# Performance work log

Measured on AMD Instinct MI355X. Metric: run time of the kernel, lower is better.

Reference implementation:

```python
import jax, jax.numpy as jnp
import numpy as np

N = 100000   # nodes
E = 1600000  # edges (before self-loops)
C = 128      # num_node_features == graph_hidden_channels (residuals require equality)
NHID = 512
NOUT = 256
B = 512      # number of graphs in the batch
BN_EPS = 1e-5


def setup_inputs() -> dict:
    key = jax.random.key(0)
    ks = list(jax.random.split(key, 32))
    k = iter(ks)

    def w(shape, fan_in):
        return jax.random.normal(next(k), shape, jnp.float32) * (1.0 / np.sqrt(fan_in))

    inp = {}
    inp["x"] = jax.random.normal(next(k), (N, C), jnp.float32)
    inp["edge_index"] = jax.random.randint(next(k), (2, E), 0, N, jnp.int32)
    inp["batch"] = jnp.sort(jax.random.randint(next(k), (N,), 0, B, jnp.int32))
    # three GCN layers: lin weight [C,C], bias [C], BN gamma/beta
    for i in (1, 2, 3):
        inp[f"W{i}"] = w((C, C), C)
        inp[f"b{i}"] = jnp.zeros((C,), jnp.float32)
        inp[f"g{i}"] = jnp.ones((C,), jnp.float32)
        inp[f"be{i}"] = jnp.zeros((C,), jnp.float32)
    # GAT (1 head)
    inp["Wa"] = w((C, C), C)
    inp["asrc"] = w((C,), C)
    inp["adst"] = w((C,), C)
    inp["ba"] = jnp.zeros((C,), jnp.float32)
    inp["ga"] = jnp.ones((C,), jnp.float32)
    inp["bea"] = jnp.zeros((C,), jnp.float32)
    # MLP head
    inp["Wh1"] = w((C, NHID), C)
    inp["bh1"] = jnp.zeros((NHID,), jnp.float32)
    inp["Wm0"] = w((NHID, NHID), NHID)
    inp["bm0"] = jnp.zeros((NHID,), jnp.float32)
    inp["Wm1"] = w((NHID, NHID), NHID)
    inp["bm1"] = jnp.zeros((NHID,), jnp.float32)
    inp["Wo"] = w((NHID, NOUT), NHID)
    inp["bo"] = jnp.zeros((NOUT,), jnp.float32)
    return inp


def _add_self_loops(edge_index):
    loops = jnp.arange(N, dtype=edge_index.dtype)
    src = jnp.concatenate([edge_index[0], loops])
    dst = jnp.concatenate([edge_index[1], loops])
    return src, dst


def _gcn(x, src, dst, W, b):
    # PyG GCNConv: add self-loops, D^-1/2 (A+I) D^-1/2 (x W) + b
    deg = jax.ops.segment_sum(jnp.ones_like(dst, jnp.float32), dst, num_segments=N)
    dinv = jax.lax.rsqrt(jnp.maximum(deg, 1.0))
    norm = dinv[src] * dinv[dst]                      # [E+N]
    h = x @ W                                         # [N,C]
    msg = h[src] * norm[:, None]                      # gather + scale
    return jax.ops.segment_sum(msg, dst, num_segments=N) + b


def _gat(x, src, dst, W, asrc, adst, b):
    # PyG GATConv, heads=1: self-loops, alpha = softmax_dst(leaky_relu(a_s.h_j + a_d.h_i))
    h = x @ W                                         # [N,C]
    es = (h * asrc).sum(-1)                           # [N]
    ed = (h * adst).sum(-1)
    e = jax.nn.leaky_relu(es[src] + ed[dst], 0.2)     # [E+N]
    m = jax.ops.segment_max(e, dst, num_segments=N)
    ex = jnp.exp(e - m[dst])
    s = jax.ops.segment_sum(ex, dst, num_segments=N)
    alpha = ex / (s[dst] + 1e-16)
    out = jax.ops.segment_sum(h[src] * alpha[:, None], dst, num_segments=N)
    return out + b


def _bn(h, g, be):
    # BatchNorm in training mode: biased batch stats over node dim
    m = h.mean(0)
    v = ((h - m) ** 2).mean(0)
    return (h - m) * jax.lax.rsqrt(v + BN_EPS) * g + be


def reference(x, edge_index, batch,
              W1, b1, g1, be1, W2, b2, g2, be2, W3, b3, g3, be3,
              Wa, asrc, adst, ba, ga, bea,
              Wh1, bh1, Wm0, bm0, Wm1, bm1, Wo, bo):
    src, dst = _add_self_loops(edge_index)
    x = jax.nn.relu(_bn(_gcn(x, src, dst, W1, b1), g1, be1)) + x
    x = jax.nn.relu(_bn(_gcn(x, src, dst, W2, b2), g2, be2)) + x
    x = jax.nn.relu(_bn(_gcn(x, src, dst, W3, b3), g3, be3)) + x
    x = jax.nn.relu(_bn(_gat(x, src, dst, Wa, asrc, adst, ba), ga, bea)) + x
    # global mean pool over graphs
    sums = jax.ops.segment_sum(x, batch, num_segments=B)
    cnt = jax.ops.segment_sum(jnp.ones((N,), jnp.float32), batch, num_segments=B)
    x = sums / jnp.maximum(cnt, 1.0)[:, None]         # [B,C]
    x = jax.nn.relu(x @ Wh1 + bh1)
    x = jax.nn.relu(x @ Wm0 + bm0)
    x = jax.nn.relu(x @ Wm1 + bm1)
    return x @ Wo + bo                                # [B,NOUT]
```

## Files before the change

### kernel.cpp

```cpp
#include <hip/hip_runtime.h>

#define N_NODES 100000
#define N_EDGES 1600000
#define CCH     128
#define BG      512
#define NHID    512
#define NOUT    256
#define BN_EPS  1e-5f

typedef __attribute__((ext_vector_type(8))) short s16x8;
typedef __attribute__((ext_vector_type(4))) float f32x4;

static __device__ __forceinline__ float leaky(float x) { return x > 0.f ? x : 0.2f * x; }
static __device__ __forceinline__ uint32_t bfr16(float x) {
  uint32_t u = __float_as_uint(x);
  u += 0x7fffu + ((u >> 16) & 1u);
  return u >> 16;
}
static __device__ __forceinline__ uint32_t pack2(float a, float b) {
  return bfr16(a) | (bfr16(b) << 16);
}
static __device__ __forceinline__ float blo(uint32_t u) { return __uint_as_float(u << 16); }
static __device__ __forceinline__ float bhi(uint32_t u) { return __uint_as_float(u & 0xffff0000u); }

__global__ void hist_kernel(const int* __restrict__ dst, int* __restrict__ indeg) {
  int e = blockIdx.x * 256 + threadIdx.x;
  if (e < N_EDGES) atomicAdd(&indeg[dst[e]], 1);
}

__global__ __launch_bounds__(256) void scan_chunks(const int* __restrict__ indeg,
                                                   int* __restrict__ rowstart,
                                                   int* __restrict__ chunksum) {
  int tid = threadIdx.x;
  int base = blockIdx.x * 1024 + tid * 4;
  int4 v;
  if (base + 3 < N_NODES) {
    v = *(const int4*)(indeg + base);
  } else {
    v.x = (base + 0 < N_NODES) ? indeg[base + 0] : 0;
    v.y = (base + 1 < N_NODES) ? indeg[base + 1] : 0;
    v.z = (base + 2 < N_NODES) ? indeg[base + 2] : 0;
    v.w = (base + 3 < N_NODES) ? indeg[base + 3] : 0;
  }
  int s = v.x + v.y + v.z + v.w;
  __shared__ int ss[256];
  ss[tid] = s;
  __syncthreads();
  for (int off = 1; off < 256; off <<= 1) {
    int t = (tid >= off) ? ss[tid - off] : 0;
    __syncthreads();
    ss[tid] += t;
    __syncthreads();
  }
  int excl = ss[tid] - s;
  if (base + 0 < N_NODES) rowstart[base + 0] = excl;
  if (base + 1 < N_NODES) rowstart[base + 1] = excl + v.x;
  if (base + 2 < N_NODES) rowstart[base + 2] = excl + v.x + v.y;
  if (base + 3 < N_NODES) rowstart[base + 3] = excl + v.x + v.y + v.z;
  if (tid == 255) chunksum[blockIdx.x] = ss[255];
}

__global__ void scan_sums(int* __restrict__ chunksum, int nch) {
  __shared__ int ss[128];
  int tid = threadIdx.x;
  int v = (tid < nch) ? chunksum[tid] : 0;
  ss[tid] = v;
  __syncthreads();
  for (int off = 1; off < 128; off <<= 1) {
    int t = (tid >= off) ? ss[tid - off] : 0;
    __syncthreads();
    ss[tid] += t;
    __syncthreads();
  }
  if (tid < nch) chunksum[tid] = ss[tid] - v;
}

__global__ void scan_add_dinv(int* __restrict__ rowstart, const int* __restrict__ chunksum,
                              const int* __restrict__ indeg, float* __restrict__ dinv) {
  int i = blockIdx.x * 256 + threadIdx.x;
  if (i < N_NODES) {
    rowstart[i] += chunksum[i >> 10];
    dinv[i] = rsqrtf((float)(indeg[i] + 1));
  } else if (i == N_NODES) {
    rowstart[N_NODES] = N_EDGES;
  }
}

__global__ void scatter_edges(const int* __restrict__ src, const int* __restrict__ dst,
                              const int* __restrict__ rowstart, int* __restrict__ cursor,
                              const float* __restrict__ dinv, int2* __restrict__ csr_sw) {
  int e = blockIdx.x * 256 + threadIdx.x;
  if (e < N_EDGES) {
    int d = dst[e];
    int s = src[e];
    int p = rowstart[d] + atomicAdd(&cursor[d], 1);
    float w = dinv[s] * dinv[d];
    csr_sw[p] = make_int2(s, __float_as_int(w));
  }
}

__global__ void prep_kernel(const float2* __restrict__ x2, uint32_t* __restrict__ xb,
                            const float* __restrict__ W1, const float* __restrict__ W2,
                            const float* __restrict__ W3, const float* __restrict__ W4,
                            unsigned short* __restrict__ Wp1, unsigned short* __restrict__ Wp2,
                            unsigned short* __restrict__ Wp3, unsigned short* __restrict__ Wp4) {
  int b = blockIdx.x;
  if (b < 25000) {
    size_t idx = (size_t)b * 256 + threadIdx.x;
    float2 v = x2[idx];
    xb[idx] = pack2(v.x, v.y);
    return;
  }
  int pb = b - 25000;
  int wsel = pb >> 3;
  int t = (pb & 7) * 256 + threadIdx.x;
  const float* W = (wsel == 0) ? W1 : (wsel == 1) ? W2 : (wsel == 2) ? W3 : W4;
  unsigned short* Wp = (wsel == 0) ? Wp1 : (wsel == 1) ? Wp2 : (wsel == 2) ? Wp3 : Wp4;
  int lane = t & 63;
  int ks = (t >> 6) & 3;
  int nt = t >> 8;
  int c = nt * 16 + (lane & 15);
  int kb = ks * 32 + (lane >> 4) * 8;
#pragma unroll
  for (int i = 0; i < 8; ++i)
    Wp[(size_t)t * 8 + i] = (unsigned short)bfr16(W[(size_t)(kb + i) * 128 + c]);
}

template <int FUSE>
__global__ __launch_bounds__(256) void gemm_mfma(uint32_t* __restrict__ xbm,
                                                 const float* __restrict__ aggf,
                                                 const float* __restrict__ stats,
                                                 const float* __restrict__ gamma,
                                                 const float* __restrict__ beta,
                                                 const unsigned short* __restrict__ Wp,
                                                 uint32_t* __restrict__ Hb,
                                                 int M) {
  __shared__ float scs[128], bcs[128];
  if (FUSE) {
    int t = threadIdx.x;
    if (t < 128) {
      const float n_inv = 1.f / (float)N_NODES;
      float m = stats[t] * n_inv;
      float v = stats[128 + t] * n_inv - m * m;
      float s = gamma[t] * rsqrtf(v + BN_EPS);
      scs[t] = s;
      bcs[t] = beta[t] - m * s;
    }
    __syncthreads();
  }
  int wave = threadIdx.x >> 6, lane = threadIdx.x & 63;
  int row0 = blockIdx.x * 128 + wave * 32;
  int r = lane & 15, g = lane >> 4;

  f32x4 acc[2][8];
#pragma unroll
  for (int mt = 0; mt < 2; ++mt)
#pragma unroll
    for (int nt = 0; nt < 8; ++nt) acc[mt][nt] = (f32x4){0.f, 0.f, 0.f, 0.f};

  s16x8 a[2][4];
#pragma unroll
  for (int mt = 0; mt < 2; ++mt) {
    int row = row0 + mt * 16 + r;
    bool v = row < M;
    if (FUSE) {
#pragma unroll
      for (int ks = 0; ks < 4; ++ks) {
        int ch = ks * 32 + g * 8;
        s16x8 af = {0, 0, 0, 0, 0, 0, 0, 0};
        if (v) {
          const float4* ap = (const float4*)(aggf + (size_t)row * 128 + ch);
          float4 a0 = ap[0], a1 = ap[1];
          uint4 xo = *(const uint4*)(xbm + (size_t)row * 64 + (ch >> 1));
          float aa[8] = {a0.x, a0.y, a0.z, a0.w, a1.x, a1.y, a1.z, a1.w};
          float xold[8] = {blo(xo.x), bhi(xo.x), blo(xo.y), bhi(xo.y),
                           blo(xo.z), bhi(xo.z), blo(xo.w), bhi(xo.w)};
          uint32_t pk[4];
#pragma unroll
          for (int jj = 0; jj < 4; ++jj) {
            float r0v = fmaxf(fmaf(aa[2 * jj],     scs[ch + 2 * jj],     bcs[ch + 2 * jj]),     0.f) + xold[2 * jj];
            float r1v = fmaxf(fmaf(aa[2 * jj + 1], scs[ch + 2 * jj + 1], bcs[ch + 2 * jj + 1]), 0.f) + xold[2 * jj + 1];
            pk[jj] = pack2(r0v, r1v);
          }
          uint4 st = make_uint4(pk[0], pk[1], pk[2], pk[3]);
          *(uint4*)(xbm + (size_t)row * 64 + (ch >> 1)) = st;
          af = *(s16x8*)&st;
        }
        a[mt][ks] = af;
      }
    } else {
      const unsigned short* ap = (const unsigned short*)xbm + (size_t)row * 128 + g * 8;
#pragma unroll
      for (int ks = 0; ks < 4; ++ks) {
        s16x8 af = {0, 0, 0, 0, 0, 0, 0, 0};
        if (v) af = *(const s16x8*)(ap + ks * 32);
        a[mt][ks] = af;
      }
    }
  }
#pragma unroll
  for (int ks = 0; ks < 4; ++ks) {
#pragma unroll
    for (int nt = 0; nt < 8; ++nt) {
      s16x8 bfr = *(const s16x8*)(Wp + ((size_t)(nt * 4 + ks) * 64 + lane) * 8);
      acc[0][nt] = __builtin_amdgcn_mfma_f32_16x16x32_bf16(a[0][ks], bfr, acc[0][nt], 0, 0, 0);
      acc[1][nt] = __builtin_amdgcn_mfma_f32_16x16x32_bf16(a[1][ks], bfr, acc[1][nt], 0, 0, 0);
    }
  }
#pragma unroll
  for (int mt = 0; mt < 2; ++mt) {
#pragma unroll
    for (int nt = 0; nt < 8; ++nt) {
#pragma unroll
      for (int reg = 0; reg < 4; ++reg) {
        float v0 = acc[mt][nt][reg];
        float v1 = __shfl_xor(v0, 1);
        int row = row0 + mt * 16 + (lane >> 4) * 4 + reg;
        int col = nt * 16 + (lane & 15);
        if (!(lane & 1) && row < M)
          Hb[(size_t)row * 64 + (col >> 1)] = pack2(v0, v1);
      }
    }
  }
}

template <int GAT>
__global__ __launch_bounds__(256) void agg_kernel(const uint2* __restrict__ Hb2,
                                                  const int* __restrict__ rowstart,
                                                  const int2* __restrict__ pack,
                                                  const float* __restrict__ dinv,
                                                  const float* __restrict__ es,
                                                  const float* __restrict__ ed,
                                                  float4* __restrict__ agg4,
                                                  float* __restrict__ stats) {
  int tid = threadIdx.x;
  int lane = tid & 63;
  int hl = lane & 31;
  int half = lane >> 5;
  int gw = (blockIdx.x * 256 + tid) >> 6;
  int nw = (gridDim.x * 256) >> 6;
  float s0 = 0, s1 = 0, s2 = 0, s3 = 0, q0 = 0, q1 = 0, q2 = 0, q3 = 0;
  for (int pi = gw; pi < N_NODES / 2; pi += nw) {
    int n = 2 * pi + half;
    int e0 = rowstart[n], e1 = rowstart[n + 1];
    int len = e1 - e0;
    int G = (len + 3) >> 2;
    int Gmax = max(G, __shfl_xor(G, 32));
    int ecl = (len > 0) ? (e1 - 1) : 0;
    float edi = 0.f, selfw, fscale = 1.f;
    if (GAT) {
      edi = ed[n];
      float wself = __expf(leaky(es[n] + edi));
      float wsum = (hl == 0) ? wself : 0.f;
      for (int e = e0 + hl; e < e1; e += 32)
        wsum += __expf(leaky(__int_as_float(pack[e].y) + edi));
#pragma unroll
      for (int off = 16; off; off >>= 1) wsum += __shfl_xor(wsum, off);
      fscale = 1.f / (wsum + 1e-16f);
      selfw = wself;
    } else {
      float di = dinv[n];
      selfw = di * di;
    }
#define EDGEW(py, ok) (GAT ? ((ok) ? __expf(leaky(__int_as_float(py) + edi)) : 0.f) \
                           : ((ok) ? __int_as_float(py) : 0.f))
    uint2 hs = Hb2[(size_t)n * 32 + hl];
    float c0 = blo(hs.x) * selfw, c1 = bhi(hs.x) * selfw;
    float c2 = blo(hs.y) * selfw, c3 = bhi(hs.y) * selfw;

    if (Gmax > 0) {
      uint2 rA0, rA1, rA2, rA3;
      float wA0, wA1, wA2, wA3;
      int iB0 = 0, iB1 = 0, iB2 = 0, iB3 = 0;
      float wB0 = 0, wB1 = 0, wB2 = 0, wB3 = 0;
      {
        int e = e0;
        int2 pa = pack[e < e1 ? e : ecl];
        int2 pb = pack[e + 1 < e1 ? e + 1 : ecl];
        int2 pc = pack[e + 2 < e1 ? e + 2 : ecl];
        int2 pd = pack[e + 3 < e1 ? e + 3 : ecl];
        wA0 = EDGEW(pa.y, e < e1);
        wA1 = EDGEW(pb.y, e + 1 < e1);
        wA2 = EDGEW(pc.y, e + 2 < e1);
        wA3 = EDGEW(pd.y, e + 3 < e1);
        rA0 = Hb2[(size_t)pa.x * 32 + hl];
        rA1 = Hb2[(size_t)pb.x * 32 + hl];
        rA2 = Hb2[(size_t)pc.x * 32 + hl];
        rA3 = Hb2[(size_t)pd.x * 32 + hl];
      }
      if (Gmax > 1) {
        int e = e0 + 4;
        int2 pa = pack[e < e1 ? e : ecl];
        int2 pb = pack[e + 1 < e1 ? e + 1 : ecl];
        int2 pc = pack[e + 2 < e1 ? e + 2 : ecl];
        int2 pd = pack[e + 3 < e1 ? e + 3 : ecl];
        iB0 = pa.x; wB0 = EDGEW(pa.y, e < e1);
        iB1 = pb.x; wB1 = EDGEW(pb.y, e + 1 < e1);
        iB2 = pc.x; wB2 = EDGEW(pc.y, e + 2 < e1);
        iB3 = pd.x; wB3 = EDGEW(pd.y, e + 3 < e1);
      }
      for (int g = 0; g < Gmax; ++g) {
        uint2 rB0, rB1, rB2, rB3;
        int nI0, nI1, nI2, nI3;
        float nw0, nw1, nw2, nw3;
        if (g + 1 < Gmax) {
          rB0 = Hb2[(size_t)iB0 * 32 + hl];
          rB1 = Hb2[(size_t)iB1 * 32 + hl];
          rB2 = Hb2[(size_t)iB2 * 32 + hl];
          rB3 = Hb2[(size_t)iB3 * 32 + hl];
        }
        if (g + 2 < Gmax) {
          int e = e0 + (g + 2) * 4;
          int2 pa = pack[e < e1 ? e : ecl];
          int2 pb = pack[e + 1 < e1 ? e + 1 : ecl];
          int2 pc = pack[e + 2 < e1 ? e + 2 : ecl];
          int2 pd = pack[e + 3 < e1 ? e + 3 : ecl];
          nI0 = pa.x; nw0 = EDGEW(pa.y, e < e1);
          nI1 = pb.x; nw1 = EDGEW(pb.y, e + 1 < e1);
          nI2 = pc.x; nw2 = EDGEW(pc.y, e + 2 < e1);
          nI3 = pd.x; nw3 = EDGEW(pd.y, e + 3 < e1);
        }
        c0 = fmaf(blo(rA0.x), wA0, c0); c1 = fmaf(bhi(rA0.x), wA0, c1);
        c2 = fmaf(blo(rA0.y), wA0, c2); c3 = fmaf(bhi(rA0.y), wA0, c3);
        c0 = fmaf(blo(rA1.x), wA1, c0); c1 = fmaf(bhi(rA1.x), wA1, c1);
        c2 = fmaf(blo(rA1.y), wA1, c2); c3 = fmaf(bhi(rA1.y), wA1, c3);
        c0 = fmaf(blo(rA2.x), wA2, c0); c1 = fmaf(bhi(rA2.x), wA2, c1);
        c2 = fmaf(blo(rA2.y), wA2, c2); c3 = fmaf(bhi(rA2.y), wA2, c3);
        c0 = fmaf(blo(rA3.x), wA3, c0); c1 = fmaf(bhi(rA3.x), wA3, c1);
        c2 = fmaf(blo(rA3.y), wA3, c2); c3 = fmaf(bhi(rA3.y), wA3, c3);
        rA0 = rB0; rA1 = rB1; rA2 = rB2; rA3 = rB3;
        wA0 = wB0; wA1 = wB1; wA2 = wB2; wA3 = wB3;
        iB0 = nI0; iB1 = nI1; iB2 = nI2; iB3 = nI3;
        wB0 = nw0; wB1 = nw1; wB2 = nw2; wB3 = nw3;
      }
    }
#undef EDGEW
    if (GAT) { c0 *= fscale; c1 *= fscale; c2 *= fscale; c3 *= fscale; }
    agg4[(size_t)n * 32 + hl] = make_float4(c0, c1, c2, c3);
    s0 += c0; s1 += c1; s2 += c2; s3 += c3;
    q0 += c0 * c0; q1 += c1 * c1; q2 += c2 * c2; q3 += c3 * c3;
  }
  s0 += __shfl_xor(s0, 32); s1 += __shfl_xor(s1, 32);
  s2 += __shfl_xor(s2, 32); s3 += __shfl_xor(s3, 32);
  q0 += __shfl_xor(q0, 32); q1 += __shfl_xor(q1, 32);
  q2 += __shfl_xor(q2, 32); q3 += __shfl_xor(q3, 32);
  __shared__ float red[4][128];
  int w = tid >> 6;
  if (half == 0) {
    red[w][4 * hl + 0] = s0; red[w][4 * hl + 1] = s1;
    red[w][4 * hl + 2] = s2; red[w][4 * hl + 3] = s3;
  }
  __syncthreads();
  if (w == 0) {
    float a = red[0][2 * lane] + red[1][2 * lane] + red[2][2 * lane] + red[3][2 * lane];
    float b = red[0][2 * lane + 1] + red[1][2 * lane + 1] + red[2][2 * lane + 1] + red[3][2 * lane + 1];
    atomicAdd(&stats[2 * lane], a);
    atomicAdd(&stats[2 * lane + 1], b);
  }
  __syncthreads();
  if (half == 0) {
    red[w][4 * hl + 0] = q0; red[w][4 * hl + 1] = q1;
    red[w][4 * hl + 2] = q2; red[w][4 * hl + 3] = q3;
  }
  __syncthreads();
  if (w == 0) {
    float a = red[0][2 * lane] + red[1][2 * lane] + red[2][2 * lane] + red[3][2 * lane];
    float b = red[0][2 * lane + 1] + red[1][2 * lane + 1] + red[2][2 * lane + 1] + red[3][2 * lane + 1];
    atomicAdd(&stats[128 + 2 * lane], a);
    atomicAdd(&stats[128 + 2 * lane + 1], b);
  }
}

__global__ __launch_bounds__(256) void compute_esed(const uint32_t* __restrict__ Hb,
                                                    const float* __restrict__ asrc,
                                                    const float* __restrict__ adst,
                                                    float* __restrict__ es, float* __restrict__ ed) {
  int lane = threadIdx.x & 63;
  int gwave = (blockIdx.x * 256 + threadIdx.x) >> 6;
  if (gwave >= N_NODES) return;
  float2 av = ((const float2*)asrc)[lane];
  float2 dv = ((const float2*)adst)[lane];
  uint32_t hv = Hb[(size_t)gwave * 64 + lane];
  float hx = blo(hv), hy = bhi(hv);
  float e_s = hx * av.x + hy * av.y;
  float e_d = hx * dv.x + hy * dv.y;
  for (int off = 32; off; off >>= 1) {
    e_s += __shfl_down(e_s, off);
    e_d += __shfl_down(e_d, off);
  }
  if (lane == 0) { es[gwave] = e_s; ed[gwave] = e_d; }
}

__global__ void gat_pack_kernel(int2* __restrict__ sw, const float* __restrict__ es) {
  int e = blockIdx.x * 256 + threadIdx.x;
  if (e < N_EDGES) {
    int2 v = sw[e];
    v.y = __float_as_int(es[v.x]);
    sw[e] = v;
  }
}

__global__ void graph_starts(const int* __restrict__ batch, int* __restrict__ gstart) {
  int n = blockIdx.x * 256 + threadIdx.x;
  if (n >= N_NODES) return;
  int b = batch[n];
  int bp = (n == 0) ? -1 : batch[n - 1];
  for (int g = bp + 1; g <= b; ++g) gstart[g] = n;
  if (n == N_NODES - 1) {
    for (int g = b + 1; g <= BG; ++g) gstart[g] = N_NODES;
  }
}

__global__ __launch_bounds__(256) void pool_bn(const float* __restrict__ aggf,
                                               const uint32_t* __restrict__ xb,
                                               const float* __restrict__ stats,
                                               const float* __restrict__ gamma,
                                               const float* __restrict__ beta,
                                               const int* __restrict__ gstart,
                                               float* __restrict__ pooled) {
  int g = blockIdx.x;
  int c = threadIdx.x & 127;
  int half = threadIdx.x >> 7;
  const float n_inv = 1.f / (float)N_NODES;
  float m = stats[c] * n_inv;
  float v = stats[128 + c] * n_inv - m * m;
  float sc = gamma[c] * rsqrtf(v + BN_EPS);
  float bc = beta[c] - m * sc;
  int s = gstart[g], e = gstart[g + 1];
  float acc = 0.f;
  for (int n = s + half; n < e; n += 2) {
    float a = aggf[(size_t)n * 128 + c];
    uint32_t u = xb[(size_t)n * 64 + (c >> 1)];
    float xo = (c & 1) ? bhi(u) : blo(u);
    acc += fmaxf(fmaf(a, sc, bc), 0.f) + xo;
  }
  __shared__ float red[256];
  red[threadIdx.x] = acc;
  __syncthreads();
  if (half == 0) {
    float vsum = red[c] + red[128 + c];
    int cnt = e - s;
    pooled[(size_t)g * 128 + c] = vsum / fmaxf((float)cnt, 1.f);
  }
}

template <int RELU, int BIAS>
__global__ __launch_bounds__(256) void gemm_f32(const float* __restrict__ A,
                                                const float* __restrict__ W,
                                                const float* __restrict__ bias,
                                                float* __restrict__ Cmat,
                                                int M, int K, int N) {
  __shared__ float As[32][128];
  __shared__ float Bs[32][128];
  int tid = threadIdx.x;
  int row0 = blockIdx.x * 128, col0 = blockIdx.y * 128;
  int tx = tid & 15, ty = tid >> 4;
  float acc[8][8];
#pragma unroll
  for (int i = 0; i < 8; ++i)
#pragma unroll
    for (int j = 0; j < 8; ++j) acc[i][j] = 0.f;

  for (int k0 = 0; k0 < K; k0 += 32) {
    {
      int r = tid >> 1;
      int kseg = (tid & 1) * 16;
      bool valid = (row0 + r) < M;
      const float* ap = A + (size_t)(row0 + r) * K + k0 + kseg;
#pragma unroll
      for (int q = 0; q < 4; ++q) {
        float4 v;
        if (valid) v = *(const float4*)(ap + q * 4);
        else { v.x = v.y = v.z = v.w = 0.f; }
        As[kseg + q * 4 + 0][r] = v.x;
        As[kseg + q * 4 + 1][r] = v.y;
        As[kseg + q * 4 + 2][r] = v.z;
        As[kseg + q * 4 + 3][r] = v.w;
      }
    }
    {
      int kk = tid >> 3;
      int seg = (tid & 7) * 16;
      const float* wp = W + (size_t)(k0 + kk) * N + col0 + seg;
#pragma unroll
      for (int q = 0; q < 4; ++q)
        *(float4*)&Bs[kk][seg + q * 4] = *(const float4*)(wp + q * 4);
    }
    __syncthreads();
#pragma unroll
    for (int kk = 0; kk < 32; ++kk) {
      float4 a0 = *(const float4*)&As[kk][ty * 4];
      float4 a1 = *(const float4*)&As[kk][64 + ty * 4];
      float4 b0 = *(const float4*)&Bs[kk][tx * 4];
      float4 b1 = *(const float4*)&Bs[kk][64 + tx * 4];
      float av[8] = {a0.x, a0.y, a0.z, a0.w, a1.x, a1.y, a1.z, a1.w};
      float bv[8] = {b0.x, b0.y, b0.z, b0.w, b1.x, b1.y, b1.z, b1.w};
#pragma unroll
      for (int i = 0; i < 8; ++i)
#pragma unroll
        for (int j = 0; j < 8; ++j) acc[i][j] = fmaf(av[i], bv[j], acc[i][j]);
    }
    __syncthreads();
  }
#pragma unroll
  for (int i = 0; i < 8; ++i) {
    int r = row0 + ((i < 4) ? (ty * 4 + i) : (64 + ty * 4 + i - 4));
    if (r >= M) continue;
#pragma unroll
    for (int j = 0; j < 8; ++j) {
      int c = col0 + ((j < 4) ? (tx * 4 + j) : (64 + tx * 4 + j - 4));
      float v = acc[i][j];
      if (BIAS) v += bias[c];
      if (RELU) v = fmaxf(v, 0.f);
      Cmat[(size_t)r * N + c] = v;
    }
  }
}

extern "C" void kernel_launch(void* const* d_in, const int* in_sizes, int n_in,
                              void* d_out, int out_size, void* d_ws, size_t ws_size,
                              hipStream_t stream) {
  const float* x_in  = (const float*)d_in[0];
  const int*   eidx  = (const int*)d_in[1];
  const int*   batch = (const int*)d_in[2];
  const float* W1 = (const float*)d_in[3];
  const float* g1 = (const float*)d_in[5];
  const float* be1 = (const float*)d_in[6];
  const float* W2 = (const float*)d_in[7];
  const float* g2 = (const float*)d_in[9];
  const float* be2 = (const float*)d_in[10];
  const float* W3 = (const float*)d_in[11];
  const float* g3 = (const float*)d_in[13];
  const float* be3 = (const float*)d_in[14];
  const float* Wa = (const float*)d_in[15];
  const float* asrc = (const float*)d_in[16];
  const float* adst = (const float*)d_in[17];
  const float* ga = (const float*)d_in[19];
  const float* bea = (const float*)d_in[20];
  const float* Wh1 = (const float*)d_in[21];
  const float* bh1 = (const float*)d_in[22];
  const float* Wm0 = (const float*)d_in[23];
  const float* bm0 = (const float*)d_in[24];
  const float* Wm1 = (const float*)d_in[25];
  const float* bm1 = (const float*)d_in[26];
  const float* Wo = (const float*)d_in[27];
  const float* bo = (const float*)d_in[28];

  const int* src = eidx;
  const int* dst = eidx + N_EDGES;

  char* p = (char*)d_ws;
  auto alloc = [&](size_t bytes) {
    char* r = p;
    p += (bytes + 255) & ~(size_t)255;
    return r;
  };
  uint32_t* Hb     = (uint32_t*)alloc((size_t)N_NODES * 64 * 4);
  uint32_t* xb     = (uint32_t*)alloc((size_t)N_NODES * 64 * 4);
  float* agg       = (float*)alloc((size_t)N_NODES * CCH * 4);
  int2*  csr_sw    = (int2*)alloc((size_t)N_EDGES * 8);
  int*   rowstart  = (int*)alloc((size_t)(N_NODES + 1) * 4);
  int*   indeg     = (int*)alloc((size_t)2 * N_NODES * 4);
  int*   cursor    = indeg + N_NODES;
  float* dinv      = (float*)alloc((size_t)N_NODES * 4);
  float* es        = (float*)alloc((size_t)N_NODES * 4);
  float* ed        = (float*)alloc((size_t)N_NODES * 4);
  int*   chunksum  = (int*)alloc(128 * 4);
  float* stats     = (float*)alloc(4 * 256 * 4);
  int*   gstart    = (int*)alloc((BG + 1) * 4);
  float* pooled    = (float*)alloc((size_t)BG * CCH * 4);
  float* m1        = (float*)alloc((size_t)BG * NHID * 4);
  float* m2        = (float*)alloc((size_t)BG * NHID * 4);
  unsigned short* Wp1 = (unsigned short*)alloc(2048 * 8 * 2);
  unsigned short* Wp2 = (unsigned short*)alloc(2048 * 8 * 2);
  unsigned short* Wp3 = (unsigned short*)alloc(2048 * 8 * 2);
  unsigned short* Wp4 = (unsigned short*)alloc(2048 * 8 * 2);

  hipMemsetAsync(indeg, 0, (size_t)2 * N_NODES * 4, stream);
  hipMemsetAsync(stats, 0, 4 * 256 * 4, stream);

  hist_kernel<<<(N_EDGES + 255) / 256, 256, 0, stream>>>(dst, indeg);
  scan_chunks<<<98, 256, 0, stream>>>(indeg, rowstart, chunksum);
  scan_sums<<<1, 128, 0, stream>>>(chunksum, 98);
  scan_add_dinv<<<(N_NODES + 256) / 256, 256, 0, stream>>>(rowstart, chunksum, indeg, dinv);
  scatter_edges<<<(N_EDGES + 255) / 256, 256, 0, stream>>>(src, dst, rowstart, cursor, dinv, csr_sw);

  prep_kernel<<<25000 + 32, 256, 0, stream>>>((const float2*)x_in, xb, W1, W2, W3, Wa,
                                              Wp1, Wp2, Wp3, Wp4);

  const int gemm_blocks_m = (N_NODES + 127) / 128;
  const int AGG_BLOCKS = 2048;

  gemm_mfma<0><<<gemm_blocks_m, 256, 0, stream>>>(xb, nullptr, nullptr, nullptr, nullptr,
                                                  Wp1, Hb, N_NODES);
  agg_kernel<0><<<AGG_BLOCKS, 256, 0, stream>>>((const uint2*)Hb, rowstart, csr_sw, dinv,
                                                nullptr, nullptr, (float4*)agg, stats + 0 * 256);
  gemm_mfma<1><<<gemm_blocks_m, 256, 0, stream>>>(xb, agg, stats + 0 * 256, g1, be1,
                                                  Wp2, Hb, N_NODES);
  agg_kernel<0><<<AGG_BLOCKS, 256, 0, stream>>>((const uint2*)Hb, rowstart, csr_sw, dinv,
                                                nullptr, nullptr, (float4*)agg, stats + 1 * 256);
  gemm_mfma<1><<<gemm_blocks_m, 256, 0, stream>>>(xb, agg, stats + 1 * 256, g2, be2,
                                                  Wp3, Hb, N_NODES);
  agg_kernel<0><<<AGG_BLOCKS, 256, 0, stream>>>((const uint2*)Hb, rowstart, csr_sw, dinv,
                                                nullptr, nullptr, (float4*)agg, stats + 2 * 256);
  gemm_mfma<1><<<gemm_blocks_m, 256, 0, stream>>>(xb, agg, stats + 2 * 256, g3, be3,
                                                  Wp4, Hb, N_NODES);
  compute_esed<<<(N_NODES + 3) / 4, 256, 0, stream>>>(Hb, asrc, adst, es, ed);
  gat_pack_kernel<<<(N_EDGES + 255) / 256, 256, 0, stream>>>(csr_sw, es);
  agg_kernel<1><<<AGG_BLOCKS, 256, 0, stream>>>((const uint2*)Hb, rowstart, csr_sw, nullptr,
                                                es, ed, (float4*)agg, stats + 3 * 256);

  graph_starts<<<(N_NODES + 255) / 256, 256, 0, stream>>>(batch, gstart);
  pool_bn<<<BG, 256, 0, stream>>>(agg, xb, stats + 3 * 256, ga, bea, gstart, pooled);

  gemm_f32<1, 1><<<dim3(4, 4), 256, 0, stream>>>(pooled, Wh1, bh1, m1, BG, CCH, NHID);
  gemm_f32<1, 1><<<dim3(4, 4), 256, 0, stream>>>(m1, Wm0, bm0, m2, BG, NHID, NHID);
  gemm_f32<1, 1><<<dim3(4, 4), 256, 0, stream>>>(m2, Wm1, bm1, m1, BG, NHID, NHID);
  gemm_f32<0, 1><<<dim3(4, 2), 256, 0, stream>>>(m1, Wo, bo, (float*)d_out, BG, NHID, NOUT);
}
```

Before: 1.158 ms.

## Pad CSR rows to multiples of four, deepen agg prefetch, use bf16 MFMA for MLP head

```diff
diff --git a/kernel.cpp b/kernel.cpp
--- a/kernel.cpp
+++ b/kernel.cpp
@@ -7,6 +7,7 @@
 #define NHID    512
 #define NOUT    256
 #define BN_EPS  1e-5f
+#define CSR_CAP (N_EDGES + 4 * N_NODES + 128)
 
 typedef __attribute__((ext_vector_type(8))) short s16x8;
 typedef __attribute__((ext_vector_type(4))) float f32x4;
@@ -42,7 +43,8 @@
     v.z = (base + 2 < N_NODES) ? indeg[base + 2] : 0;
     v.w = (base + 3 < N_NODES) ? indeg[base + 3] : 0;
   }
-  int s = v.x + v.y + v.z + v.w;
+  int px = (v.x + 3) & ~3, py = (v.y + 3) & ~3, pz = (v.z + 3) & ~3, pw = (v.w + 3) & ~3;
+  int s = px + py + pz + pw;
   __shared__ int ss[256];
   ss[tid] = s;
   __syncthreads();
@@ -54,13 +56,13 @@
   }
   int excl = ss[tid] - s;
   if (base + 0 < N_NODES) rowstart[base + 0] = excl;
-  if (base + 1 < N_NODES) rowstart[base + 1] = excl + v.x;
-  if (base + 2 < N_NODES) rowstart[base + 2] = excl + v.x + v.y;
-  if (base + 3 < N_NODES) rowstart[base + 3] = excl + v.x + v.y + v.z;
+  if (base + 1 < N_NODES) rowstart[base + 1] = excl + px;
+  if (base + 2 < N_NODES) rowstart[base + 2] = excl + px + py;
+  if (base + 3 < N_NODES) rowstart[base + 3] = excl + px + py + pz;
   if (tid == 255) chunksum[blockIdx.x] = ss[255];
 }
 
-__global__ void scan_sums(int* __restrict__ chunksum, int nch) {
+__global__ void scan_sums(int* __restrict__ chunksum, int nch, int* __restrict__ totalp) {
   __shared__ int ss[128];
   int tid = threadIdx.x;
   int v = (tid < nch) ? chunksum[tid] : 0;
@@ -73,6 +75,7 @@
     __syncthreads();
   }
   if (tid < nch) chunksum[tid] = ss[tid] - v;
+  if (tid == nch - 1) *totalp = ss[tid];
 }
 
 __global__ void scan_add_dinv(int* __restrict__ rowstart, const int* __restrict__ chunksum,
@@ -81,8 +84,6 @@
   if (i < N_NODES) {
     rowstart[i] += chunksum[i >> 10];
     dinv[i] = rsqrtf((float)(indeg[i] + 1));
-  } else if (i == N_NODES) {
-    rowstart[N_NODES] = N_EDGES;
   }
 }
 
@@ -124,6 +125,30 @@
 #pragma unroll
   for (int i = 0; i < 8; ++i)
     Wp[(size_t)t * 8 + i] = (unsigned short)bfr16(W[(size_t)(kb + i) * 128 + c]);
+}
+
+__global__ void pack_mlp(const float* __restrict__ Wh1, const float* __restrict__ Wm0,
+                         const float* __restrict__ Wm1, const float* __restrict__ Wo,
+                         unsigned short* __restrict__ P1, unsigned short* __restrict__ P2,
+                         unsigned short* __restrict__ P3, unsigned short* __restrict__ P4) {
+  int t = blockIdx.x * 256 + threadIdx.x;
+  const float* W;
+  unsigned short* P;
+  int K, N, loc;
+  if (t < 8192)        { W = Wh1; P = P1; K = 128; N = 512; loc = t; }
+  else if (t < 40960)  { W = Wm0; P = P2; K = 512; N = 512; loc = t - 8192; }
+  else if (t < 73728)  { W = Wm1; P = P3; K = 512; N = 512; loc = t - 40960; }
+  else if (t < 90112)  { W = Wo;  P = P4; K = 512; N = 256; loc = t - 73728; }
+  else return;
+  int ksn = K >> 5;
+  int lane = loc & 63;
+  int ks = (loc >> 6) & (ksn - 1);
+  int nt = loc / (64 * ksn);
+  int c = nt * 16 + (lane & 15);
+  int kb = ks * 32 + (lane >> 4) * 8;
+#pragma unroll
+  for (int i = 0; i < 8; ++i)
+    P[(size_t)loc * 8 + i] = (unsigned short)bfr16(W[(size_t)(kb + i) * N + c]);
 }
 
 template <int FUSE>
@@ -224,15 +249,74 @@
   }
 }
 
+template <int RELU, int OUTF32>
+__global__ __launch_bounds__(256) void gemm_mlp(const uint32_t* __restrict__ Ab,
+                                                const unsigned short* __restrict__ Wp,
+                                                const float* __restrict__ bias,
+                                                void* __restrict__ outp,
+                                                int M, int K, int N) {
+  int wave = threadIdx.x >> 6, lane = threadIdx.x & 63;
+  int row0 = blockIdx.x * 128 + wave * 32;
+  int colb = blockIdx.y;
+  const unsigned short* A16 = (const unsigned short*)Ab;
+  int KS = K >> 5;
+  int r = lane & 15, g = lane >> 4;
+  f32x4 acc[2][8];
+#pragma unroll
+  for (int mt = 0; mt < 2; ++mt)
+#pragma unroll
+    for (int nt = 0; nt < 8; ++nt) acc[mt][nt] = (f32x4){0.f, 0.f, 0.f, 0.f};
+
+  for (int ks = 0; ks < KS; ++ks) {
+    s16x8 a[2];
+#pragma unroll
+    for (int mt = 0; mt < 2; ++mt) {
+      int row = row0 + mt * 16 + r;
+      s16x8 af = {0, 0, 0, 0, 0, 0, 0, 0};
+      if (row < M) af = *(const s16x8*)(A16 + (size_t)row * K + ks * 32 + g * 8);
+      a[mt] = af;
+    }
+#pragma unroll
+    for (int ntl = 0; ntl < 8; ++ntl) {
+      int ntg = colb * 8 + ntl;
+      s16x8 b = *(const s16x8*)(Wp + ((size_t)(ntg * KS + ks) * 64 + lane) * 8);
+      acc[0][ntl] = __builtin_amdgcn_mfma_f32_16x16x32_bf16(a[0], b, acc[0][ntl], 0, 0, 0);
+      acc[1][ntl] = __builtin_amdgcn_mfma_f32_16x16x32_bf16(a[1], b, acc[1][ntl], 0, 0, 0);
+    }
+  }
+#pragma unroll
+  for (int mt = 0; mt < 2; ++mt) {
+#pragma unroll
+    for (int ntl = 0; ntl < 8; ++ntl) {
+#pragma unroll
+      for (int reg = 0; reg < 4; ++reg) {
+        int row = row0 + mt * 16 + (lane >> 4) * 4 + reg;
+        int col = colb * 128 + ntl * 16 + (lane & 15);
+        float v0 = acc[mt][ntl][reg] + bias[col];
+        if (RELU) v0 = fmaxf(v0, 0.f);
+        if (OUTF32) {
+          if (row < M) ((float*)outp)[(size_t)row * N + col] = v0;
+        } else {
+          float v1 = __shfl_xor(v0, 1);
+          if (!(lane & 1) && row < M)
+            ((uint32_t*)outp)[(size_t)row * (N >> 1) + (col >> 1)] = pack2(v0, v1);
+        }
+      }
+    }
+  }
+}
+
 template <int GAT>
 __global__ __launch_bounds__(256) void agg_kernel(const uint2* __restrict__ Hb2,
                                                   const int* __restrict__ rowstart,
                                                   const int2* __restrict__ pack,
                                                   const float* __restrict__ dinv,
+                                                  const int* __restrict__ indeg,
                                                   const float* __restrict__ es,
                                                   const float* __restrict__ ed,
                                                   float4* __restrict__ agg4,
                                                   float* __restrict__ stats) {
+  const float INVALW = GAT ? -1e30f : 0.0f;
   int tid = threadIdx.x;
   int lane = tid & 63;
   int hl = lane & 31;
@@ -240,19 +324,30 @@
   int gw = (blockIdx.x * 256 + tid) >> 6;
   int nw = (gridDim.x * 256) >> 6;
   float s0 = 0, s1 = 0, s2 = 0, s3 = 0, q0 = 0, q1 = 0, q2 = 0, q3 = 0;
+
+#define LOADPK(gq, I0, I1, I2, I3, V0, V1, V2, V3)                        \
+  do {                                                                    \
+    bool ok = (gq) < G;                                                   \
+    int ee = e0 + (gq) * 4;                                               \
+    int2 pa = pack[ee], pb = pack[ee + 1], pc = pack[ee + 2], pd = pack[ee + 3]; \
+    I0 = ok ? pa.x : 0; V0 = ok ? __int_as_float(pa.y) : INVALW;          \
+    I1 = ok ? pb.x : 0; V1 = ok ? __int_as_float(pb.y) : INVALW;          \
+    I2 = ok ? pc.x : 0; V2 = ok ? __int_as_float(pc.y) : INVALW;          \
+    I3 = ok ? pd.x : 0; V3 = ok ? __int_as_float(pd.y) : INVALW;          \
+  } while (0)
+
   for (int pi = gw; pi < N_NODES / 2; pi += nw) {
     int n = 2 * pi + half;
-    int e0 = rowstart[n], e1 = rowstart[n + 1];
-    int len = e1 - e0;
-    int G = (len + 3) >> 2;
+    int e0 = rowstart[n], e1p = rowstart[n + 1];
+    int G = (e1p - e0) >> 2;
     int Gmax = max(G, __shfl_xor(G, 32));
-    int ecl = (len > 0) ? (e1 - 1) : 0;
     float edi = 0.f, selfw, fscale = 1.f;
     if (GAT) {
+      int len = indeg[n];
       edi = ed[n];
       float wself = __expf(leaky(es[n] + edi));
       float wsum = (hl == 0) ? wself : 0.f;
-      for (int e = e0 + hl; e < e1; e += 32)
+      for (int e = e0 + hl; e < e0 + len; e += 32)
         wsum += __expf(leaky(__int_as_float(pack[e].y) + edi));
 #pragma unroll
       for (int off = 16; off; off >>= 1) wsum += __shfl_xor(wsum, off);
@@ -262,84 +357,73 @@
       float di = dinv[n];
       selfw = di * di;
     }
-#define EDGEW(py, ok) (GAT ? ((ok) ? __expf(leaky(__int_as_float(py) + edi)) : 0.f) \
-                           : ((ok) ? __int_as_float(py) : 0.f))
     uint2 hs = Hb2[(size_t)n * 32 + hl];
     float c0 = blo(hs.x) * selfw, c1 = bhi(hs.x) * selfw;
     float c2 = blo(hs.y) * selfw, c3 = bhi(hs.y) * selfw;
 
     if (Gmax > 0) {
-      uint2 rA0, rA1, rA2, rA3;
+      int j0, j1, j2, j3;
+      float wC0, wC1, wC2, wC3;
+      float wB0, wB1, wB2, wB3;
       float wA0, wA1, wA2, wA3;
-      int iB0 = 0, iB1 = 0, iB2 = 0, iB3 = 0;
-      float wB0 = 0, wB1 = 0, wB2 = 0, wB3 = 0;
-      {
-        int e = e0;
-        int2 pa = pack[e < e1 ? e : ecl];
-        int2 pb = pack[e + 1 < e1 ? e + 1 : ecl];
-        int2 pc = pack[e + 2 < e1 ? e + 2 : ecl];
-        int2 pd = pack[e + 3 < e1 ? e + 3 : ecl];
-        wA0 = EDGEW(pa.y, e < e1);
-        wA1 = EDGEW(pb.y, e + 1 < e1);
-        wA2 = EDGEW(pc.y, e + 2 < e1);
-        wA3 = EDGEW(pd.y, e + 3 < e1);
-        rA0 = Hb2[(size_t)pa.x * 32 + hl];
-        rA1 = Hb2[(size_t)pb.x * 32 + hl];
-        rA2 = Hb2[(size_t)pc.x * 32 + hl];
-        rA3 = Hb2[(size_t)pd.x * 32 + hl];
+      uint2 R00, R01, R02, R03;
+      uint2 R10, R11, R12, R13;
+      LOADPK(0, j0, j1, j2, j3, wC0, wC1, wC2, wC3);
+      R00 = Hb2[(size_t)(unsigned)j0 * 32 + hl];
+      R01 = Hb2[(size_t)(unsigned)j1 * 32 + hl];
+      R02 = Hb2[(size_t)(unsigned)j2 * 32 + hl];
+      R03 = Hb2[(size_t)(unsigned)j3 * 32 + hl];
+      LOADPK(1, j0, j1, j2, j3, wB0, wB1, wB2, wB3);
+      R10 = Hb2[(size_t)(unsigned)j0 * 32 + hl];
+      R11 = Hb2[(size_t)(unsigned)j1 * 32 + hl];
+      R12 = Hb2[(size_t)(unsigned)j2 * 32 + hl];
+      R13 = Hb2[(size_t)(unsigned)j3 * 32 + hl];
+      LOADPK(2, j0, j1, j2, j3, wA0, wA1, wA2, wA3);
+      for (int g = 0; g < Gmax; ++g) {
+        uint2 R20, R21, R22, R23;
+        if (g + 2 < Gmax) {
+          R20 = Hb2[(size_t)(unsigned)j0 * 32 + hl];
+          R21 = Hb2[(size_t)(unsigned)j1 * 32 + hl];
+          R22 = Hb2[(size_t)(unsigned)j2 * 32 + hl];
+          R23 = Hb2[(size_t)(unsigned)j3 * 32 + hl];
+        }
+        int k0, k1, k2, k3;
+        float wN0, wN1, wN2, wN3;
+        if (g + 3 < Gmax) {
+          LOADPK(g + 3, k0, k1, k2, k3, wN0, wN1, wN2, wN3);
+        } else {
+          k0 = k1 = k2 = k3 = 0;
+          wN0 = wN1 = wN2 = wN3 = INVALW;
+        }
+        float f0, f1, f2, f3;
+        if (GAT) {
+          f0 = __expf(leaky(wC0 + edi)); f1 = __expf(leaky(wC1 + edi));
+          f2 = __expf(leaky(wC2 + edi)); f3 = __expf(leaky(wC3 + edi));
+        } else {
+          f0 = wC0; f1 = wC1; f2 = wC2; f3 = wC3;
+        }
+        c0 = fmaf(blo(R00.x), f0, c0); c1 = fmaf(bhi(R00.x), f0, c1);
+        c2 = fmaf(blo(R00.y), f0, c2); c3 = fmaf(bhi(R00.y), f0, c3);
+        c0 = fmaf(blo(R01.x), f1, c0); c1 = fmaf(bhi(R01.x), f1, c1);
+        c2 = fmaf(blo(R01.y), f1, c2); c3 = fmaf(bhi(R01.y), f1, c3);
+        c0 = fmaf(blo(R02.x), f2, c0); c1 = fmaf(bhi(R02.x), f2, c1);
+        c2 = fmaf(blo(R02.y), f2, c2); c3 = fmaf(bhi(R02.y), f2, c3);
+        c0 = fmaf(blo(R03.x), f3, c0); c1 = fmaf(bhi(R03.x), f3, c1);
+        c2 = fmaf(blo(R03.y), f3, c2); c3 = fmaf(bhi(R03.y), f3, c3);
+        R00 = R10; R01 = R11; R02 = R12; R03 = R13;
+        R10 = R20; R11 = R21; R12 = R22; R13 = R23;
+        wC0 = wB0; wC1 = wB1; wC2 = wB2; wC3 = wB3;
+        wB0 = wA0; wB1 = wA1; wB2 = wA2; wB3 = wA3;
+        wA0 = wN0; wA1 = wN1; wA2 = wN2; wA3 = wN3;
+        j0 = k0; j1 = k1; j2 = k2; j3 = k3;
       }
-      if (Gmax > 1) {
-        int e = e0 + 4;
-        int2 pa = pack[e < e1 ? e : ecl];
-        int2 pb = pack[e + 1 < e1 ? e + 1 : ecl];
-        int2 pc = pack[e + 2 < e1 ? e + 2 : ecl];
-        int2 pd = pack[e + 3 < e1 ? e + 3 : ecl];
-        iB0 = pa.x; wB0 = EDGEW(pa.y, e < e1);
-        iB1 = pb.x; wB1 = EDGEW(pb.y, e + 1 < e1);
-        iB2 = pc.x; wB2 = EDGEW(pc.y, e + 2 < e1);
-        iB3 = pd.x; wB3 = EDGEW(pd.y, e + 3 < e1);
-      }
-      for (int g = 0; g < Gmax; ++g) {
-        uint2 rB0, rB1, rB2, rB3;
-        int nI0, nI1, nI2, nI3;
-        float nw0, nw1, nw2, nw3;
-        if (g + 1 < Gmax) {
-          rB0 = Hb2[(size_t)iB0 * 32 + hl];
-          rB1 = Hb2[(size_t)iB1 * 32 + hl];
-          rB2 = Hb2[(size_t)iB2 * 32 + hl];
-          rB3 = Hb2[(size_t)iB3 * 32 + hl];
-        }
-        if (g + 2 < Gmax) {
-          int e = e0 + (g + 2) * 4;
-          int2 pa = pack[e < e1 ? e : ecl];
-          int2 pb = pack[e + 1 < e1 ? e + 1 : ecl];
-          int2 pc = pack[e + 2 < e1 ? e + 2 : ecl];
-          int2 pd = pack[e + 3 < e1 ? e + 3 : ecl];
-          nI0 = pa.x; nw0 = EDGEW(pa.y, e < e1);
-          nI1 = pb.x; nw1 = EDGEW(pb.y, e + 1 < e1);
-          nI2 = pc.x; nw2 = EDGEW(pc.y, e + 2 < e1);
-          nI3 = pd.x; nw3 = EDGEW(pd.y, e + 3 < e1);
-        }
-        c0 = fmaf(blo(rA0.x), wA0, c0); c1 = fmaf(bhi(rA0.x), wA0, c1);
-        c2 = fmaf(blo(rA0.y), wA0, c2); c3 = fmaf(bhi(rA0.y), wA0, c3);
-        c0 = fmaf(blo(rA1.x), wA1, c0); c1 = fmaf(bhi(rA1.x), wA1, c1);
-        c2 = fmaf(blo(rA1.y), wA1, c2); c3 = fmaf(bhi(rA1.y), wA1, c3);
-        c0 = fmaf(blo(rA2.x), wA2, c0); c1 = fmaf(bhi(rA2.x), wA2, c1);
-        c2 = fmaf(blo(rA2.y), wA2, c2); c3 = fmaf(bhi(rA2.y), wA2, c3);
-        c0 = fmaf(blo(rA3.x), wA3, c0); c1 = fmaf(bhi(rA3.x), wA3, c1);
-        c2 = fmaf(blo(rA3.y), wA3, c2); c3 = fmaf(bhi(rA3.y), wA3, c3);
-        rA0 = rB0; rA1 = rB1; rA2 = rB2; rA3 = rB3;
-        wA0 = wB0; wA1 = wB1; wA2 = wB2; wA3 = wB3;
-        iB0 = nI0; iB1 = nI1; iB2 = nI2; iB3 = nI3;
-        wB0 = nw0; wB1 = nw1; wB2 = nw2; wB3 = nw3;
-      }
-    }
-#undef EDGEW
+    }
     if (GAT) { c0 *= fscale; c1 *= fscale; c2 *= fscale; c3 *= fscale; }
     agg4[(size_t)n * 32 + hl] = make_float4(c0, c1, c2, c3);
     s0 += c0; s1 += c1; s2 += c2; s3 += c3;
     q0 += c0 * c0; q1 += c1 * c1; q2 += c2 * c2; q3 += c3 * c3;
   }
+#undef LOADPK
   s0 += __shfl_xor(s0, 32); s1 += __shfl_xor(s1, 32);
   s2 += __shfl_xor(s2, 32); s3 += __shfl_xor(s3, 32);
   q0 += __shfl_xor(q0, 32); q1 += __shfl_xor(q1, 32);
@@ -393,9 +477,9 @@
 
 __global__ void gat_pack_kernel(int2* __restrict__ sw, const float* __restrict__ es) {
   int e = blockIdx.x * 256 + threadIdx.x;
-  if (e < N_EDGES) {
+  if (e < CSR_CAP) {
     int2 v = sw[e];
-    v.y = __float_as_int(es[v.x]);
+    v.y = (v.y == 0) ? __float_as_int(-1e30f) : __float_as_int(es[v.x]);
     sw[e] = v;
   }
 }
@@ -417,7 +501,7 @@
                                                const float* __restrict__ gamma,
                                                const float* __restrict__ beta,
                                                const int* __restrict__ gstart,
-                                               float* __restrict__ pooled) {
+                                               uint32_t* __restrict__ pooledb) {
   int g = blockIdx.x;
   int c = threadIdx.x & 127;
   int half = threadIdx.x >> 7;
@@ -435,86 +519,17 @@
     acc += fmaxf(fmaf(a, sc, bc), 0.f) + xo;
   }
   __shared__ float red[256];
+  __shared__ float fin[128];
   red[threadIdx.x] = acc;
   __syncthreads();
   if (half == 0) {
     float vsum = red[c] + red[128 + c];
     int cnt = e - s;
-    pooled[(size_t)g * 128 + c] = vsum / fmaxf((float)cnt, 1.f);
-  }
-}
-
-template <int RELU, int BIAS>
-__global__ __launch_bounds__(256) void gemm_f32(const float* __restrict__ A,
-                                                const float* __restrict__ W,
-                                                const float* __restrict__ bias,
-                                                float* __restrict__ Cmat,
-                                                int M, int K, int N) {
-  __shared__ float As[32][128];
-  __shared__ float Bs[32][128];
-  int tid = threadIdx.x;
-  int row0 = blockIdx.x * 128, col0 = blockIdx.y * 128;
-  int tx = tid & 15, ty = tid >> 4;
-  float acc[8][8];
-#pragma unroll
-  for (int i = 0; i < 8; ++i)
-#pragma unroll
-    for (int j = 0; j < 8; ++j) acc[i][j] = 0.f;
-
-  for (int k0 = 0; k0 < K; k0 += 32) {
-    {
-      int r = tid >> 1;
-      int kseg = (tid & 1) * 16;
-      bool valid = (row0 + r) < M;
-      const float* ap = A + (size_t)(row0 + r) * K + k0 + kseg;
-#pragma unroll
-      for (int q = 0; q < 4; ++q) {
-        float4 v;
-        if (valid) v = *(const float4*)(ap + q * 4);
-        else { v.x = v.y = v.z = v.w = 0.f; }
-        As[kseg + q * 4 + 0][r] = v.x;
-        As[kseg + q * 4 + 1][r] = v.y;
-        As[kseg + q * 4 + 2][r] = v.z;
-        As[kseg + q * 4 + 3][r] = v.w;
-      }
-    }
-    {
-      int kk = tid >> 3;
-      int seg = (tid & 7) * 16;
-      const float* wp = W + (size_t)(k0 + kk) * N + col0 + seg;
-#pragma unroll
-      for (int q = 0; q < 4; ++q)
-        *(float4*)&Bs[kk][seg + q * 4] = *(const float4*)(wp + q * 4);
-    }
-    __syncthreads();
-#pragma unroll
-    for (int kk = 0; kk < 32; ++kk) {
-      float4 a0 = *(const float4*)&As[kk][ty * 4];
-      float4 a1 = *(const float4*)&As[kk][64 + ty * 4];
-      float4 b0 = *(const float4*)&Bs[kk][tx * 4];
-      float4 b1 = *(const float4*)&Bs[kk][64 + tx * 4];
-      float av[8] = {a0.x, a0.y, a0.z, a0.w, a1.x, a1.y, a1.z, a1.w};
-      float bv[8] = {b0.x, b0.y, b0.z, b0.w, b1.x, b1.y, b1.z, b1.w};
-#pragma unroll
-      for (int i = 0; i < 8; ++i)
-#pragma unroll
-        for (int j = 0; j < 8; ++j) acc[i][j] = fmaf(av[i], bv[j], acc[i][j]);
-    }
-    __syncthreads();
-  }
-#pragma unroll
-  for (int i = 0; i < 8; ++i) {
-    int r = row0 + ((i < 4) ? (ty * 4 + i) : (64 + ty * 4 + i - 4));
-    if (r >= M) continue;
-#pragma unroll
-    for (int j = 0; j < 8; ++j) {
-      int c = col0 + ((j < 4) ? (tx * 4 + j) : (64 + tx * 4 + j - 4));
-      float v = acc[i][j];
-      if (BIAS) v += bias[c];
-      if (RELU) v = fmaxf(v, 0.f);
-      Cmat[(size_t)r * N + c] = v;
-    }
-  }
+    fin[c] = vsum / fmaxf((float)cnt, 1.f);
+  }
+  __syncthreads();
+  if (half == 0 && !(c & 1))
+    pooledb[(size_t)g * 64 + (c >> 1)] = pack2(fin[c], fin[c + 1]);
 }
 
 extern "C" void kernel_launch(void* const* d_in, const int* in_sizes, int n_in,
@@ -558,7 +573,7 @@
   uint32_t* Hb     = (uint32_t*)alloc((size_t)N_NODES * 64 * 4);
   uint32_t* xb     = (uint32_t*)alloc((size_t)N_NODES * 64 * 4);
   float* agg       = (float*)alloc((size_t)N_NODES * CCH * 4);
-  int2*  csr_sw    = (int2*)alloc((size_t)N_EDGES * 8);
+  int2*  csr_sw    = (int2*)alloc((size_t)CSR_CAP * 8);
   int*   rowstart  = (int*)alloc((size_t)(N_NODES + 1) * 4);
   int*   indeg     = (int*)alloc((size_t)2 * N_NODES * 4);
   int*   cursor    = indeg + N_NODES;
@@ -568,25 +583,31 @@
   int*   chunksum  = (int*)alloc(128 * 4);
   float* stats     = (float*)alloc(4 * 256 * 4);
   int*   gstart    = (int*)alloc((BG + 1) * 4);
-  float* pooled    = (float*)alloc((size_t)BG * CCH * 4);
-  float* m1        = (float*)alloc((size_t)BG * NHID * 4);
-  float* m2        = (float*)alloc((size_t)BG * NHID * 4);
+  uint32_t* pooledb = (uint32_t*)alloc((size_t)BG * 64 * 4);
+  uint32_t* m1b    = (uint32_t*)alloc((size_t)BG * (NHID / 2) * 4);
+  uint32_t* m2b    = (uint32_t*)alloc((size_t)BG * (NHID / 2) * 4);
   unsigned short* Wp1 = (unsigned short*)alloc(2048 * 8 * 2);
   unsigned short* Wp2 = (unsigned short*)alloc(2048 * 8 * 2);
   unsigned short* Wp3 = (unsigned short*)alloc(2048 * 8 * 2);
   unsigned short* Wp4 = (unsigned short*)alloc(2048 * 8 * 2);
+  unsigned short* P1 = (unsigned short*)alloc((size_t)8192 * 8 * 2);
+  unsigned short* P2 = (unsigned short*)alloc((size_t)32768 * 8 * 2);
+  unsigned short* P3 = (unsigned short*)alloc((size_t)32768 * 8 * 2);
+  unsigned short* P4 = (unsigned short*)alloc((size_t)16384 * 8 * 2);
 
   hipMemsetAsync(indeg, 0, (size_t)2 * N_NODES * 4, stream);
   hipMemsetAsync(stats, 0, 4 * 256 * 4, stream);
+  hipMemsetAsync(csr_sw, 0, (size_t)CSR_CAP * 8, stream);
 
   hist_kernel<<<(N_EDGES + 255) / 256, 256, 0, stream>>>(dst, indeg);
   scan_chunks<<<98, 256, 0, stream>>>(indeg, rowstart, chunksum);
-  scan_sums<<<1, 128, 0, stream>>>(chunksum, 98);
-  scan_add_dinv<<<(N_NODES + 256) / 256, 256, 0, stream>>>(rowstart, chunksum, indeg, dinv);
+  scan_sums<<<1, 128, 0, stream>>>(chunksum, 98, rowstart + N_NODES);
+  scan_add_dinv<<<(N_NODES + 255) / 256, 256, 0, stream>>>(rowstart, chunksum, indeg, dinv);
   scatter_edges<<<(N_EDGES + 255) / 256, 256, 0, stream>>>(src, dst, rowstart, cursor, dinv, csr_sw);
 
   prep_kernel<<<25000 + 32, 256, 0, stream>>>((const float2*)x_in, xb, W1, W2, W3, Wa,
                                               Wp1, Wp2, Wp3, Wp4);
+  pack_mlp<<<352, 256, 0, stream>>>(Wh1, Wm0, Wm1, Wo, P1, P2, P3, P4);
 
   const int gemm_blocks_m = (N_NODES + 127) / 128;
   const int AGG_BLOCKS = 2048;
@@ -594,27 +615,27 @@
   gemm_mfma<0><<<gemm_blocks_m, 256, 0, stream>>>(xb, nullptr, nullptr, nullptr, nullptr,
                                                   Wp1, Hb, N_NODES);
   agg_kernel<0><<<AGG_BLOCKS, 256, 0, stream>>>((const uint2*)Hb, rowstart, csr_sw, dinv,
-                                                nullptr, nullptr, (float4*)agg, stats + 0 * 256);
+                                                indeg, nullptr, nullptr, (float4*)agg, stats + 0 * 256);
   gemm_mfma<1><<<gemm_blocks_m, 256, 0, stream>>>(xb, agg, stats + 0 * 256, g1, be1,
                                                   Wp2, Hb, N_NODES);
   agg_kernel<0><<<AGG_BLOCKS, 256, 0, stream>>>((const uint2*)Hb, rowstart, csr_sw, dinv,
-                                                nullptr, nullptr, (float4*)agg, stats + 1 * 256);
+                                                indeg, nullptr, nullptr, (float4*)agg, stats + 1 * 256);
   gemm_mfma<1><<<gemm_blocks_m, 256, 0, stream>>>(xb, agg, stats + 1 * 256, g2, be2,
                                                   Wp3, Hb, N_NODES);
   agg_kernel<0><<<AGG_BLOCKS, 256, 0, stream>>>((const uint2*)Hb, rowstart, csr_sw, dinv,
-                                                nullptr, nullptr, (float4*)agg, stats + 2 * 256);
+                                                indeg, nullptr, nullptr, (float4*)agg, stats + 2 * 256);
   gemm_mfma<1><<<gemm_blocks_m, 256, 0, stream>>>(xb, agg, stats + 2 * 256, g3, be3,
                                                   Wp4, Hb, N_NODES);
   compute_esed<<<(N_NODES + 3) / 4, 256, 0, stream>>>(Hb, asrc, adst, es, ed);
-  gat_pack_kernel<<<(N_EDGES + 255) / 256, 256, 0, stream>>>(csr_sw, es);
+  gat_pack_kernel<<<(CSR_CAP + 255) / 256, 256, 0, stream>>>(csr_sw, es);
   agg_kernel<1><<<AGG_BLOCKS, 256, 0, stream>>>((const uint2*)Hb, rowstart, csr_sw, nullptr,
-                                                es, ed, (float4*)agg, stats + 3 * 256);
+                                                indeg, es, ed, (float4*)agg, stats + 3 * 256);
 
   graph_starts<<<(N_NODES + 255) / 256, 256, 0, stream>>>(batch, gstart);
-  pool_bn<<<BG, 256, 0, stream>>>(agg, xb, stats + 3 * 256, ga, bea, gstart, pooled);
-
-  gemm_f32<1, 1><<<dim3(4, 4), 256, 0, stream>>>(pooled, Wh1, bh1, m1, BG, CCH, NHID);
-  gemm_f32<1, 1><<<dim3(4, 4), 256, 0, stream>>>(m1, Wm0, bm0, m2, BG, NHID, NHID);
-  gemm_f32<1, 1><<<dim3(4, 4), 256, 0, stream>>>(m2, Wm1, bm1, m1, BG, NHID, NHID);
-  gemm_f32<0, 1><<<dim3(4, 2), 256, 0, stream>>>(m1, Wo, bo, (float*)d_out, BG, NHID, NOUT);
-}
+  pool_bn<<<BG, 256, 0, stream>>>(agg, xb, stats + 3 * 256, ga, bea, gstart, pooledb);
+
+  gemm_mlp<1, 0><<<dim3(4, 4), 256, 0, stream>>>(pooledb, P1, bh1, m1b, BG, CCH, NHID);
+  gemm_mlp<1, 0><<<dim3(4, 4), 256, 0, stream>>>(m1b, P2, bm0, m2b, BG, NHID, NHID);
+  gemm_mlp<1, 0><<<dim3(4, 4), 256, 0, stream>>>(m2b, P3, bm1, m1b, BG, NHID, NHID);
+  gemm_mlp<0, 1><<<dim3(4, 2), 256, 0, stream>>>(m1b, P4, bo, d_out, BG, NHID, NOUT);
+}
```

After: 1.041 ms. 1.11x faster.
